# Kernel tuning notes

Hardware: AMD Instinct MI355X
Metric: run time of the kernel (lower is better)

The kernel has to match this reference:

```python
import jax, jax.numpy as jnp
import numpy as np
import math

B, Q_LEN, D, H, KV = 8, 2048, 1024, 16, 256
HD = D // H

def setup_inputs() -> dict:
    key0 = jax.random.key(0)
    ks = jax.random.split(key0, 6)
    query = jax.random.normal(ks[0], (B, Q_LEN, D), dtype=jnp.float32)
    key = jax.random.normal(ks[1], (B, 1024), dtype=jnp.float32)
    value = jax.random.normal(ks[2], (B, 1024), dtype=jnp.float32)
    clip_score = jax.random.uniform(ks[3], (B, KV), dtype=jnp.float32)
    # k_linear / v_linear weights (embed_dim, 1024), no bias
    k_weight = jax.random.normal(ks[4], (D, 1024), dtype=jnp.float32) * 0.02
    v_weight = jax.random.normal(ks[5], (D, 1024), dtype=jnp.float32) * 0.02
    # scale_linear: Linear(512, 1), weight const 0.05, bias const 7.5 (per nn.init.constant_)
    scale_w = jnp.full((2 * KV,), 0.05, dtype=jnp.float32)
    scale_b = jnp.array(7.5, dtype=jnp.float32)
    return {"query": query, "key": key, "value": value, "clip_score": clip_score,
            "k_weight": k_weight, "v_weight": v_weight, "scale_w": scale_w, "scale_b": scale_b}

def reference(query, key, value, clip_score, k_weight, v_weight, scale_w, scale_b):
    act_scale = 1.0
    b, qlen, d = query.shape
    # key/value are (B,1024): expand to (B,KV,1024) as in torch branch
    key_e = jnp.broadcast_to(key[:, None, :], (b, KV, key.shape[-1]))
    val_e = jnp.broadcast_to(value[:, None, :], (b, KV, value.shape[-1]))
    K = jnp.einsum('bkc,dc->bkd', key_e, k_weight)   # (B,KV,D)
    V = jnp.einsum('bkc,dc->bkd', val_e, v_weight)   # (B,KV,D)
    Qh = query.reshape(b, qlen, H, HD).transpose(0, 2, 1, 3)  # (B,H,Q,HD)
    Kh = K.reshape(b, KV, H, HD).transpose(0, 2, 1, 3)        # (B,H,KV,HD)
    Vh = V.reshape(b, KV, H, HD).transpose(0, 2, 1, 3)        # (B,H,KV,HD)
    scores = jnp.einsum('bhqd,bhkd->bhqk', Qh, Kh) / math.sqrt(HD)  # (B,H,Q,KV)
    # scale_linear(cat([scores, clip], -1)) == scores@w1 + clip@w2 + b (avoid materializing concat)
    w1, w2 = scale_w[:KV], scale_w[KV:]
    lin = (jnp.einsum('bhqk,k->bhq', scores, w1)[..., None]
           + (clip_score @ w2)[:, None, None, None] + scale_b)   # (B,H,Q,1)
    clip_e = clip_score[:, None, None, :]                        # (B,1,1,KV)
    scores = scores + (lin * clip_e) * act_scale
    attn_weights = jax.nn.softmax(scores, axis=-1)
    out = jnp.einsum('bhqk,bhkd->bhqd', attn_weights, Vh)
    out = out.transpose(0, 2, 1, 3).reshape(b, qlen, d)
    return (out, attn_weights)
```

## Files before the change

kernel.cpp:

```cpp
#include <hip/hip_runtime.h>
#include <hip/hip_bf16.h>

#define B_    8
#define QLEN  2048
#define D_    1024
#define H_    16
#define KV_   256
#define HD_   64

typedef float fvec4 __attribute__((ext_vector_type(4)));

#define WS_KVEC 0
#define WS_VVEC 8192
#define WS_C2   16384
#define WS_SW1  16392

__device__ inline float wave_sum(float v) {
#pragma unroll
  for (int off = 32; off > 0; off >>= 1) v += __shfl_xor(v, off, 64);
  return v;
}
__device__ inline float wave_max(float v) {
#pragma unroll
  for (int off = 32; off > 0; off >>= 1) v = fmaxf(v, __shfl_xor(v, off, 64));
  return v;
}
__device__ inline float wave_min(float v) {
#pragma unroll
  for (int off = 32; off > 0; off >>= 1) v = fminf(v, __shfl_xor(v, off, 64));
  return v;
}

template <int N>
__device__ inline void multi_sum(float* v) {
#pragma unroll
  for (int off = 32; off > 0; off >>= 1) {
#pragma unroll
    for (int r = 0; r < N; ++r) v[r] += __shfl_xor(v[r], off, 64);
  }
}

__global__ __launch_bounds__(256) void prep_kernel(
    const float* __restrict__ key, const float* __restrict__ value,
    const float* __restrict__ kw, const float* __restrict__ vw,
    const float* __restrict__ clip, const float* __restrict__ scale_w,
    float* __restrict__ ws) {
  const int lane = threadIdx.x & 63;
  const int waveId = threadIdx.x >> 6;

  if (blockIdx.x == 1024) {
    if (waveId != 0) return;
    const float4* sw4 = reinterpret_cast<const float4*>(scale_w);
    float4 a = sw4[lane];
    float s = wave_sum(a.x + a.y + a.z + a.w);
    if (lane == 0) ws[WS_SW1] = s;
    float4 w2 = sw4[64 + lane];
    for (int b = 0; b < B_; ++b) {
      const float4* c4 = reinterpret_cast<const float4*>(clip + b * KV_);
      float4 c = c4[lane];
      float p = c.x * w2.x + c.y * w2.y + c.z * w2.z + c.w * w2.w;
      p = wave_sum(p);
      if (lane == 0) ws[WS_C2 + b] = p;
    }
    return;
  }

  const int W = blockIdx.x * 4 + waveId;
  const int sel = W >> 11;
  const int rem = W & 2047;
  const int b = rem >> 8;
  const int g = rem & 255;
  const float* x = (sel ? value : key) + b * 1024;
  const float* Wt = sel ? vw : kw;
  const float4* x4 = reinterpret_cast<const float4*>(x);
  float4 xs[4];
#pragma unroll
  for (int i = 0; i < 4; ++i) xs[i] = x4[i * 64 + lane];
  float* outv = ws + (sel ? WS_VVEC : WS_KVEC) + b * 1024;
  float acc[4];
#pragma unroll
  for (int r = 0; r < 4; ++r) {
    const int d = g * 4 + r;
    const float4* w4 = reinterpret_cast<const float4*>(Wt + (size_t)d * 1024);
    acc[r] = 0.f;
#pragma unroll
    for (int i = 0; i < 4; ++i) {
      float4 w = w4[i * 64 + lane];
      acc[r] += xs[i].x * w.x + xs[i].y * w.y + xs[i].z * w.z + xs[i].w * w.w;
    }
  }
  multi_sum<4>(acc);
  if (lane < 4) outv[g * 4 + lane] = acc[lane];
}

__global__ __launch_bounds__(256) void attn_kernel(
    const float* __restrict__ query, const float* __restrict__ clip,
    const float* __restrict__ scale_b, const float* __restrict__ ws,
    float* __restrict__ attn, float* __restrict__ out) {
  const int lane = threadIdx.x & 63;
  const int waveId = threadIdx.x >> 6;
  const int rowBase = blockIdx.x * 64 + waveId * 16;
  const int b = rowBase >> 15;
  const int h = (rowBase >> 11) & 15;
  const int q0 = rowBase & 2047;

  {
    const fvec4* v4 = reinterpret_cast<const fvec4*>(ws + WS_VVEC);
    fvec4* o4 = reinterpret_cast<fvec4*>(out);
    const int idx = blockIdx.x * 256 + threadIdx.x;
#pragma unroll
    for (int i = 0; i < 4; ++i) {
      const int j = idx + i * 1048576;
      const int ob = j >> 19;
      const int d4 = j & 255;
      fvec4 v = v4[ob * 256 + d4];
      __builtin_nontemporal_store(v, &o4[j]);
    }
  }

  const float kv = ws[WS_KVEC + b * 1024 + h * 64 + lane];
  const float4* c4 = reinterpret_cast<const float4*>(clip + b * KV_);
  const float4 cl = c4[lane];
  const float cmax = wave_max(fmaxf(fmaxf(cl.x, cl.y), fmaxf(cl.z, cl.w)));
  const float cmin = wave_min(fminf(fminf(cl.x, cl.y), fminf(cl.z, cl.w)));
  const float sw1 = ws[WS_SW1];
  const float Lc = ws[WS_C2 + b] + scale_b[0];

  const float* qbase = query + ((size_t)(b * QLEN + q0)) * D_ + h * HD_ + lane;
  float qv[16];
#pragma unroll
  for (int r = 0; r < 16; ++r) qv[r] = __builtin_nontemporal_load(&qbase[(size_t)r * D_]);

  float sp[16];
#pragma unroll
  for (int r = 0; r < 16; ++r) sp[r] = qv[r] * kv;
  multi_sum<16>(sp);

  float L[16], m[16];
#pragma unroll
  for (int r = 0; r < 16; ++r) {
    L[r] = sw1 * (sp[r] * 0.125f) + Lc;
    m[r] = (L[r] >= 0.f) ? L[r] * cmax : L[r] * cmin;
  }

  float dp[16];
#pragma unroll
  for (int r = 0; r < 16; ++r) {
    dp[r] = __expf(L[r] * cl.x - m[r]) + __expf(L[r] * cl.y - m[r]) +
            __expf(L[r] * cl.z - m[r]) + __expf(L[r] * cl.w - m[r]);
  }
  multi_sum<16>(dp);

  fvec4* a4 = reinterpret_cast<fvec4*>(attn) + (size_t)rowBase * 64 + lane;
#pragma unroll
  for (int r = 0; r < 16; ++r) {
    const float rd = 1.0f / dp[r];
    fvec4 e;
    e.x = __expf(L[r] * cl.x - m[r]) * rd;
    e.y = __expf(L[r] * cl.y - m[r]) * rd;
    e.z = __expf(L[r] * cl.z - m[r]) * rd;
    e.w = __expf(L[r] * cl.w - m[r]) * rd;
    __builtin_nontemporal_store(e, &a4[(size_t)r * 64]);
  }
}

extern "C" void kernel_launch(void* const* d_in, const int* in_sizes, int n_in,
                              void* d_out, int out_size, void* d_ws, size_t ws_size,
                              hipStream_t stream) {
  const float* query   = (const float*)d_in[0];
  const float* key     = (const float*)d_in[1];
  const float* value   = (const float*)d_in[2];
  const float* clip    = (const float*)d_in[3];
  const float* kw      = (const float*)d_in[4];
  const float* vw      = (const float*)d_in[5];
  const float* scale_w = (const float*)d_in[6];
  const float* scale_b = (const float*)d_in[7];
  float* out  = (float*)d_out;
  float* attn = out + (size_t)B_ * QLEN * D_;
  float* ws   = (float*)d_ws;

  hipLaunchKernelGGL(prep_kernel, dim3(1025), dim3(256), 0, stream,
                     key, value, kw, vw, clip, scale_w, ws);
  hipLaunchKernelGGL(attn_kernel, dim3(4096), dim3(256), 0, stream,
                     query, clip, scale_b, ws, attn, out);
}
```

Measured before the change: 87.48 us.

## Split attention into query-dot kernel and separate softmax/output streaming kernel

The fused attention kernel is split in two. The first kernel computes the per-row scale L with float4 query loads and 16-lane reductions, then writes it to workspace. The second kernel loops over 32 rows per wave, computing the softmax with one wave reduction per row, and streams both the attention weights and the broadcast output. The aim is to separate the query-read phase from the write-heavy phase and to cut register pressure from the 16-row arrays. The cost is an extra kernel launch and a workspace round trip, and the second kernel runs fewer, longer-lived waves.

Result: faster. 82.93 us (-5.2%).

```diff
diff --git a/kernel.cpp b/kernel.cpp
--- a/kernel.cpp
+++ b/kernel.cpp
@@ -14,6 +14,7 @@
 #define WS_VVEC 8192
 #define WS_C2   16384
 #define WS_SW1  16392
+#define WS_L    16400
 
 __device__ inline float wave_sum(float v) {
 #pragma unroll
@@ -30,7 +31,6 @@
   for (int off = 32; off > 0; off >>= 1) v = fminf(v, __shfl_xor(v, off, 64));
   return v;
 }
-
 template <int N>
 __device__ inline void multi_sum(float* v) {
 #pragma unroll
@@ -93,74 +93,78 @@
   if (lane < 4) outv[g * 4 + lane] = acc[lane];
 }
 
-__global__ __launch_bounds__(256) void attn_kernel(
-    const float* __restrict__ query, const float* __restrict__ clip,
-    const float* __restrict__ scale_b, const float* __restrict__ ws,
-    float* __restrict__ attn, float* __restrict__ out) {
+__global__ __launch_bounds__(256) void qdot_kernel(
+    const float* __restrict__ query, const float* __restrict__ scale_b,
+    float* __restrict__ ws) {
   const int lane = threadIdx.x & 63;
   const int waveId = threadIdx.x >> 6;
   const int rowBase = blockIdx.x * 64 + waveId * 16;
   const int b = rowBase >> 15;
   const int h = (rowBase >> 11) & 15;
   const int q0 = rowBase & 2047;
+  const int g = lane >> 4;
+  const int c = lane & 15;
 
-  {
-    const fvec4* v4 = reinterpret_cast<const fvec4*>(ws + WS_VVEC);
-    fvec4* o4 = reinterpret_cast<fvec4*>(out);
-    const int idx = blockIdx.x * 256 + threadIdx.x;
-#pragma unroll
-    for (int i = 0; i < 4; ++i) {
-      const int j = idx + i * 1048576;
-      const int ob = j >> 19;
-      const int d4 = j & 255;
-      fvec4 v = v4[ob * 256 + d4];
-      __builtin_nontemporal_store(v, &o4[j]);
-    }
-  }
-
-  const float kv = ws[WS_KVEC + b * 1024 + h * 64 + lane];
-  const float4* c4 = reinterpret_cast<const float4*>(clip + b * KV_);
-  const float4 cl = c4[lane];
-  const float cmax = wave_max(fmaxf(fmaxf(cl.x, cl.y), fmaxf(cl.z, cl.w)));
-  const float cmin = wave_min(fminf(fminf(cl.x, cl.y), fminf(cl.z, cl.w)));
+  const fvec4 kvv = reinterpret_cast<const fvec4*>(ws + WS_KVEC + b * 1024 + h * HD_)[c];
   const float sw1 = ws[WS_SW1];
   const float Lc = ws[WS_C2 + b] + scale_b[0];
 
-  const float* qbase = query + ((size_t)(b * QLEN + q0)) * D_ + h * HD_ + lane;
-  float qv[16];
+  const float* qb = query + ((size_t)(b * QLEN + q0)) * D_ + h * HD_;
+  float p[4];
 #pragma unroll
-  for (int r = 0; r < 16; ++r) qv[r] = __builtin_nontemporal_load(&qbase[(size_t)r * D_]);
+  for (int j = 0; j < 4; ++j) {
+    const fvec4 q4 = __builtin_nontemporal_load(
+        reinterpret_cast<const fvec4*>(qb + (size_t)(j * 4 + g) * D_) + c);
+    p[j] = q4.x * kvv.x + q4.y * kvv.y + q4.z * kvv.z + q4.w * kvv.w;
+  }
+#pragma unroll
+  for (int off = 1; off <= 8; off <<= 1) {
+#pragma unroll
+    for (int j = 0; j < 4; ++j) p[j] += __shfl_xor(p[j], off, 64);
+  }
+  if (c < 4) {
+    const float sp = (c == 0) ? p[0] : (c == 1) ? p[1] : (c == 2) ? p[2] : p[3];
+    ws[WS_L + rowBase + c * 4 + g] = sw1 * (sp * 0.125f) + Lc;
+  }
+}
 
-  float sp[16];
-#pragma unroll
-  for (int r = 0; r < 16; ++r) sp[r] = qv[r] * kv;
-  multi_sum<16>(sp);
+__global__ __launch_bounds__(256) void stream_kernel(
+    const float* __restrict__ clip, const float* __restrict__ ws,
+    float* __restrict__ attn, float* __restrict__ out) {
+  const int lane = threadIdx.x & 63;
+  const int gwave = (blockIdx.x * 256 + threadIdx.x) >> 6;
+  const int row0 = gwave * 32;
+  const int b = row0 >> 15;
 
-  float L[16], m[16];
-#pragma unroll
-  for (int r = 0; r < 16; ++r) {
-    L[r] = sw1 * (sp[r] * 0.125f) + Lc;
-    m[r] = (L[r] >= 0.f) ? L[r] * cmax : L[r] * cmin;
+  const fvec4 cl = reinterpret_cast<const fvec4*>(clip + b * KV_)[lane];
+  const float cmax = wave_max(fmaxf(fmaxf(cl.x, cl.y), fmaxf(cl.z, cl.w)));
+  const float cmin = wave_min(fminf(fminf(cl.x, cl.y), fminf(cl.z, cl.w)));
+  const float* Lp = ws + WS_L + row0;
+
+  fvec4* a4 = reinterpret_cast<fvec4*>(attn) + (size_t)row0 * 64 + lane;
+#pragma unroll 4
+  for (int i = 0; i < 32; ++i) {
+    const float Ld = Lp[i];
+    const float m = (Ld >= 0.f) ? Ld * cmax : Ld * cmin;
+    fvec4 e;
+    e.x = __expf(Ld * cl.x - m);
+    e.y = __expf(Ld * cl.y - m);
+    e.z = __expf(Ld * cl.z - m);
+    e.w = __expf(Ld * cl.w - m);
+    const float den = wave_sum(e.x + e.y + e.z + e.w);
+    e *= (1.0f / den);
+    __builtin_nontemporal_store(e, &a4[(size_t)i * 64]);
   }
 
-  float dp[16];
+  const fvec4* v4 = reinterpret_cast<const fvec4*>(ws + WS_VVEC);
+  fvec4* o4 = reinterpret_cast<fvec4*>(out);
 #pragma unroll
-  for (int r = 0; r < 16; ++r) {
-    dp[r] = __expf(L[r] * cl.x - m[r]) + __expf(L[r] * cl.y - m[r]) +
-            __expf(L[r] * cl.z - m[r]) + __expf(L[r] * cl.w - m[r]);
-  }
-  multi_sum<16>(dp);
-
-  fvec4* a4 = reinterpret_cast<fvec4*>(attn) + (size_t)rowBase * 64 + lane;
-#pragma unroll
-  for (int r = 0; r < 16; ++r) {
-    const float rd = 1.0f / dp[r];
-    fvec4 e;
-    e.x = __expf(L[r] * cl.x - m[r]) * rd;
-    e.y = __expf(L[r] * cl.y - m[r]) * rd;
-    e.z = __expf(L[r] * cl.z - m[r]) * rd;
-    e.w = __expf(L[r] * cl.w - m[r]) * rd;
-    __builtin_nontemporal_store(e, &a4[(size_t)r * 64]);
+  for (int i = 0; i < 8; ++i) {
+    const int j = (gwave * 8 + i) * 64 + lane;
+    const int ob = j >> 19;
+    const int d4 = j & 255;
+    fvec4 v = v4[ob * 256 + d4];
+    __builtin_nontemporal_store(v, &o4[j]);
   }
 }
 
@@ -181,6 +185,8 @@
 
   hipLaunchKernelGGL(prep_kernel, dim3(1025), dim3(256), 0, stream,
                      key, value, kw, vw, clip, scale_w, ws);
-  hipLaunchKernelGGL(attn_kernel, dim3(4096), dim3(256), 0, stream,
-                     query, clip, scale_b, ws, attn, out);
+  hipLaunchKernelGGL(qdot_kernel, dim3(4096), dim3(256), 0, stream,
+                     query, scale_b, ws);
+  hipLaunchKernelGGL(stream_kernel, dim3(2048), dim3(256), 0, stream,
+                     clip, ws, attn, out);
 }
```
